# Performance work log

Hardware: AMD Instinct MI355X
Metric: run time of the kernel (lower is better)

## Reference

```python
import jax, jax.numpy as jnp
import numpy as np

B, N, IN, HID, OUT = 64, 256, 7, 64, 32
DEG = 32
NT = B * N          # total nodes per side
E = NT * DEG        # intra-graph edges per side
TAU = 1.0
MAX_ITER = 10
EPS = 1e-5          # InstanceNorm2d eps


def setup_inputs() -> dict:
    key = jax.random.key(0)
    ks = jax.random.split(key, 12)

    def edges(k):
        # random intra-graph edges: local indices in [0, N) plus per-graph offset
        loc = jax.random.randint(k, (2, B, N * DEG), 0, N)
        off = (jnp.arange(B) * N)[None, :, None]
        return (loc + off).reshape(2, -1).astype(jnp.int64)

    def lin(k, fi, fo):
        return jax.random.normal(k, (fi, fo), jnp.float32) / np.float32(np.sqrt(fi))

    return {
        "x1": jax.random.normal(ks[0], (NT, IN), jnp.float32),
        "x2": jax.random.normal(ks[1], (NT, IN), jnp.float32),
        "edge1": edges(ks[2]),
        "edge2": edges(ks[3]),
        "Wl1": lin(ks[4], IN, HID), "Wr1": lin(ks[5], IN, HID),
        "bl1": jnp.zeros((HID,), jnp.float32), "br1": jnp.zeros((HID,), jnp.float32),
        "att1": jax.random.normal(ks[6], (HID,), jnp.float32) * 0.1,
        "bias1": jnp.zeros((HID,), jnp.float32),
        "Wl2": lin(ks[7], HID, OUT), "Wr2": lin(ks[8], HID, OUT),
        "bl2": jnp.zeros((OUT,), jnp.float32), "br2": jnp.zeros((OUT,), jnp.float32),
        "att2": jax.random.normal(ks[9], (OUT,), jnp.float32) * 0.1,
        "bias2": jnp.zeros((OUT,), jnp.float32),
        "gamma": jnp.ones((1,), jnp.float32),
        "beta": jnp.zeros((1,), jnp.float32),
    }


def _gatv2(x, src, dst, Wl, bl, Wr, br, att, bias):
    # PyG GATv2Conv, heads=1: score = att . leaky_relu(lin_l(x_j) + lin_r(x_i))
    xl = x @ Wl + bl  # source transform
    xr = x @ Wr + br  # target transform
    e = jax.nn.leaky_relu(xl[src] + xr[dst], 0.2)     # [E, D]
    score = e @ att                                    # [E]
    smax = jax.ops.segment_max(score, dst, num_segments=NT)
    ex = jnp.exp(score - smax[dst])
    den = jax.ops.segment_sum(ex, dst, num_segments=NT)
    alpha = ex / den[dst]
    out = jax.ops.segment_sum(alpha[:, None] * xl[src], dst, num_segments=NT)
    return out + bias


def _encode(x, edge, params):
    # add self loops (PyG add_self_loops=True default)
    loops = jnp.arange(NT)
    src = jnp.concatenate([edge[0], loops])
    dst = jnp.concatenate([edge[1], loops])
    h = jax.nn.relu(_gatv2(x, src, dst, *params[0]))
    return _gatv2(h, src, dst, *params[1])


def _soft_topk(sim_n):
    # AFAT-style differentiable top-k: OT between flattened scores and
    # {min, max} anchors with marginals [(n-k)/n, k/n], k = N2 per pair.
    n = N * N
    k = N
    flat = sim_n.reshape(B, n)
    mn = flat.min(axis=1, keepdims=True)
    mx = flat.max(axis=1, keepdims=True)
    dist = jnp.stack([flat - mn, mx - flat], axis=-1)  # [B, n, 2] (|s-min|,|s-max|)
    logK = -dist / TAU
    log_row = -jnp.log(jnp.float32(n))
    log_col = jnp.log(jnp.array([(n - k) / n, k / n], jnp.float32))
    for i in range(MAX_ITER):
        if i % 2 == 0:  # row normalization to uniform 1/n
            logK = logK - jax.scipy.special.logsumexp(logK, axis=-1, keepdims=True) + log_row
        else:           # column normalization to [(n-k)/n, k/n]
            logK = logK - jax.scipy.special.logsumexp(logK, axis=1, keepdims=True) + log_col[None, None, :]
    soft = jnp.clip(jnp.exp(logK[:, :, 1]) * n, 0.0, 1.0)  # selection probability per entry
    return soft.reshape(B, N, N)


def reference(x1, x2, edge1, edge2, Wl1, Wr1, bl1, br1, att1, bias1,
              Wl2, Wr2, bl2, br2, att2, bias2, gamma, beta):
    params = ((Wl1, bl1, Wr1, br1, att1, bias1), (Wl2, bl2, Wr2, br2, att2, bias2))
    h1 = _encode(x1, edge1, params).reshape(B, N, OUT)
    h2 = _encode(x2, edge2, params).reshape(B, N, OUT)
    sim = jnp.einsum('bnd,bmd->bnm', h1, h2)
    # InstanceNorm2d(1, affine=True): normalize each pair's sim matrix
    mu = sim.mean(axis=(1, 2), keepdims=True)
    var = sim.var(axis=(1, 2), keepdims=True)
    sim_n = gamma[0] * (sim - mu) * jax.lax.rsqrt(var + EPS) + beta[0]
    return _soft_topk(sim_n)  # soft_S stacked over the batch, [B, N, N]
```

## Files before the change

kernel.cpp:

```cpp
#include <hip/hip_runtime.h>

#define NB 64
#define NN 256
#define IND 7
#define HIDD 64
#define OUTD 32
#define EPG 8192
#define ETOT 524288
#define CAPQ 2600
#define SRCPAD 2624

typedef _Float16 f16;
typedef f16 f16x2 __attribute__((ext_vector_type(2)));
typedef f16 f16x4 __attribute__((ext_vector_type(4)));
typedef f16 f16x8 __attribute__((ext_vector_type(8)));
typedef float f32x4 __attribute__((ext_vector_type(4)));

__device__ __forceinline__ float bsum16(float v, float* rb){
#pragma unroll
  for (int o = 32; o > 0; o >>= 1) v += __shfl_xor(v, o, 64);
  __syncthreads();
  if ((threadIdx.x & 63) == 0) rb[threadIdx.x >> 6] = v;
  __syncthreads();
  float s = 0.f;
#pragma unroll
  for (int i = 0; i < 16; i++) s += rb[i];
  return s;
}
__device__ __forceinline__ float bmin16(float v, float* rb){
#pragma unroll
  for (int o = 32; o > 0; o >>= 1) v = fminf(v, __shfl_xor(v, o, 64));
  __syncthreads();
  if ((threadIdx.x & 63) == 0) rb[threadIdx.x >> 6] = v;
  __syncthreads();
  float s = rb[0];
#pragma unroll
  for (int i = 1; i < 16; i++) s = fminf(s, rb[i]);
  return s;
}
__device__ __forceinline__ float bmax16(float v, float* rb){
#pragma unroll
  for (int o = 32; o > 0; o >>= 1) v = fmaxf(v, __shfl_xor(v, o, 64));
  __syncthreads();
  if ((threadIdx.x & 63) == 0) rb[threadIdx.x >> 6] = v;
  __syncthreads();
  float s = rb[0];
#pragma unroll
  for (int i = 1; i < 16; i++) s = fmaxf(s, rb[i]);
  return s;
}

__device__ __forceinline__ f16x2 lrelu2(f16x2 s){
  const f16x2 k = {(f16)0.2f, (f16)0.2f};
  return __builtin_elementwise_max(s, s * k);
}
__device__ __forceinline__ f16x2 shfl_h2(f16x2 v, int lane){
  int i = __builtin_bit_cast(int, v);
  i = __shfl(i, lane, 64);
  return __builtin_bit_cast(f16x2, i);
}
__device__ __forceinline__ unsigned fkey(float f){
  unsigned b = __float_as_uint(f);
  return (b & 0x80000000u) ? ~b : (b | 0x80000000u);
}
__device__ __forceinline__ float fkinv(unsigned k){
  unsigned b = (k & 0x80000000u) ? (k ^ 0x80000000u) : ~k;
  return __uint_as_float(b);
}

__global__ __launch_bounds__(512, 4) void gat1(
    const float* __restrict__ x1, const float* __restrict__ x2,
    const int* __restrict__ e1, const int* __restrict__ e2,
    const float* __restrict__ Wl, const float* __restrict__ Wr,
    const float* __restrict__ bl, const float* __restrict__ br,
    const float* __restrict__ att, const float* __restrict__ bias,
    f16* __restrict__ hmid,
    int* __restrict__ meta, unsigned char* __restrict__ srcs)
{
  __shared__ __align__(16) f16 xl_s[256 * 72];
  __shared__ float sc_s[CAPQ];
  __shared__ unsigned int src_su[SRCPAD / 4];
  __shared__ int deg_s[64], start_s[64], cnt_s[64];
  __shared__ unsigned char perm[64];
  unsigned char* src_s = (unsigned char*)src_su;

  const int bid = blockIdx.x;
  const int gs = bid >> 2, lo = (bid & 3) * 64;
  const int side = gs >> 6, g = gs & 63;
  const float* x = side ? x2 : x1;
  const int* eb = side ? e2 : e1;
  const int* es = eb + g * EPG;
  const int* ed = eb + ETOT + g * EPG;
  const int t = threadIdx.x;

  if (t < 64) deg_s[t] = 0;

  unsigned short epk[17];
  int nE = 0;
#pragma unroll
  for (int i = 0; i < 17; i++){
    int e = t + i * 512;
    if (e < EPG + 256){
      int sl, dl;
      if (e < EPG){ sl = es[e] & 255; dl = ed[e] & 255; }
      else { sl = dl = e - EPG; }
      epk[i] = (unsigned short)((dl << 8) | sl);
      nE = i + 1;
    }
  }

  {
    const int node = t >> 1, dh = t & 1;
    float xv[IND];
    const float* xr_ = x + (g * 256 + node) * IND;
#pragma unroll
    for (int k = 0; k < IND; k++) xv[k] = xr_[k];
#pragma unroll
    for (int ch = 0; ch < 4; ch++){
      f16x8 o;
#pragma unroll
      for (int j = 0; j < 8; j++){
        int dd = dh * 32 + ch * 8 + j;
        float a = bl[dd];
#pragma unroll
        for (int k = 0; k < IND; k++) a = fmaf(xv[k], Wl[k * HIDD + dd], a);
        o[j] = (f16)a;
      }
      *(f16x8*)&xl_s[node * 72 + dh * 32 + ch * 8] = o;
    }
  }
  __syncthreads();

#pragma unroll
  for (int i = 0; i < 17; i++) if (i < nE){
    int r = (epk[i] >> 8) - lo;
    if ((unsigned)r < 64u) atomicAdd(&deg_s[r], 1);
  }
  __syncthreads();
  if (t < 64){
    int v = deg_s[t], s = v;
#pragma unroll
    for (int off = 1; off < 64; off <<= 1){
      int u = __shfl_up(s, off, 64);
      if (t >= off) s += u;
    }
    start_s[t] = s - v;
    cnt_s[t] = s - v;
    meta[bid * 128 + t] = s - v;
    meta[bid * 128 + 64 + t] = v;
    int r = 0;
#pragma unroll 8
    for (int j = 0; j < 64; j++){
      int dj = deg_s[j];
      r += (dj < v) || (dj == v && j < t);
    }
    perm[r] = (unsigned char)t;
  }
  __syncthreads();
#pragma unroll
  for (int i = 0; i < 17; i++) if (i < nE){
    int dl = epk[i] >> 8, r = dl - lo;
    if ((unsigned)r < 64u){
      int p = atomicAdd(&cnt_s[r], 1);
      if (p < CAPQ) src_s[p] = (unsigned char)(epk[i] & 255);
    }
  }
  __syncthreads();
  {
    int ttl = start_s[63] + deg_s[63];
    if (ttl > CAPQ) ttl = CAPQ;
    unsigned int* gsrc = (unsigned int*)(srcs + (size_t)bid * SRCPAD);
    int nw = (ttl + 3) >> 2;
    for (int i = t; i < nw; i += 512) gsrc[i] = src_su[i];
  }

  const int pairi = perm[t >> 3], sub = t & 7, ln = lo + pairi;
  f16x2 m[4], am[4];
  {
    float xv[IND];
    const float* xq = x + (g * 256 + ln) * IND;
#pragma unroll
    for (int k = 0; k < IND; k++) xv[k] = xq[k];
#pragma unroll
    for (int c = 0; c < 4; c++){
#pragma unroll
      for (int u = 0; u < 2; u++){
        int dd = sub * 8 + 2 * c + u;
        float a = br[dd];
#pragma unroll
        for (int k = 0; k < IND; k++) a = fmaf(xv[k], Wr[k * HIDD + dd], a);
        m[c][u] = (f16)a;
        am[c][u] = (f16)att[dd];
      }
    }
  }
  f16x2 xrh[32], atth[32];
  {
    const int base = (t & 63) & ~7;
#pragma unroll
    for (int ss = 0; ss < 8; ss++){
#pragma unroll
      for (int c = 0; c < 4; c++){
        xrh[ss * 4 + c] = shfl_h2(m[c], base + ss);
        atth[ss * 4 + c] = shfl_h2(am[c], base + ss);
      }
    }
  }

  const int s0 = start_s[pairi];
  int sE = s0 + deg_s[pairi];
  if (sE > CAPQ) sE = CAPQ;
  float lmax = -3.0e38f;
  for (int idx = s0 + sub; idx < sE; idx += 8){
    int sl = src_s[idx];
    const f16x8* rp = (const f16x8*)&xl_s[(unsigned)sl * 72];
    float accs[4] = {0.f, 0.f, 0.f, 0.f};
#pragma unroll
    for (int blk = 0; blk < 8; blk++){
      f16x8 rv = rp[blk];
#pragma unroll
      for (int u = 0; u < 4; u++){
        f16x2 v = {rv[2 * u], rv[2 * u + 1]};
        v = v + xrh[blk * 4 + u];
        accs[u] = __builtin_amdgcn_fdot2(lrelu2(v), atth[blk * 4 + u], accs[u], false);
      }
    }
    float sc = (accs[0] + accs[1]) + (accs[2] + accs[3]);
    sc_s[idx] = sc;
    lmax = fmaxf(lmax, sc);
  }
  lmax = fmaxf(lmax, __shfl_xor(lmax, 1, 64));
  lmax = fmaxf(lmax, __shfl_xor(lmax, 2, 64));
  lmax = fmaxf(lmax, __shfl_xor(lmax, 4, 64));
  const float smax = lmax;
  float ssum = 0.f;
  for (int idx = s0 + sub; idx < sE; idx += 8){
    float w = __expf(sc_s[idx] - smax);
    ssum += w;
    sc_s[idx] = w;
  }
  ssum += __shfl_xor(ssum, 1, 64);
  ssum += __shfl_xor(ssum, 2, 64);
  ssum += __shfl_xor(ssum, 4, 64);
  float inv = 1.f / ssum;
  float acc[8];
#pragma unroll
  for (int c = 0; c < 8; c++) acc[c] = 0.f;
  {
    int sl = (s0 < sE) ? src_s[s0] : 0;
    f16x8 row = *(const f16x8*)&xl_s[(unsigned)sl * 72 + sub * 8];
    for (int idx = s0; idx < sE; idx++){
      int sln = (idx + 1 < sE) ? src_s[idx + 1] : 0;
      f16x8 rown = *(const f16x8*)&xl_s[(unsigned)sln * 72 + sub * 8];
      float w = sc_s[idx];
#pragma unroll
      for (int c = 0; c < 8; c++) acc[c] = fmaf(w, (float)row[c], acc[c]);
      row = rown;
    }
  }
  f16x8 o;
#pragma unroll
  for (int c = 0; c < 8; c++)
    o[c] = (f16)fmaxf(acc[c] * inv + bias[sub * 8 + c], 0.f);
  *(f16x8*)(hmid + (size_t)(gs * 256 + ln) * 64 + sub * 8) = o;
}

__global__ __launch_bounds__(512, 4) void gat2(
    const int* __restrict__ meta, const unsigned char* __restrict__ srcs,
    const f16* __restrict__ hmid,
    const float* __restrict__ Wl, const float* __restrict__ Wr,
    const float* __restrict__ bl, const float* __restrict__ br,
    const float* __restrict__ att, const float* __restrict__ bias,
    f16* __restrict__ hout)
{
  __shared__ __align__(16) f16 xl_s[256 * 40];
  __shared__ __align__(16) f16 xr_s[64 * 40];
  __shared__ float sc_s[CAPQ];
  __shared__ unsigned int src_su[SRCPAD / 4];
  __shared__ int start_s[64], deg_s[64];
  __shared__ unsigned char perm[64];
  unsigned char* src_s = (unsigned char*)src_su;

  const int bid = blockIdx.x;
  const int gs = bid >> 2, lo = (bid & 3) * 64;
  const int t = threadIdx.x;

  if (t < 64){
    start_s[t] = meta[bid * 128 + t];
    deg_s[t] = meta[bid * 128 + 64 + t];
  }
  {
    int ttl = meta[bid * 128 + 63] + meta[bid * 128 + 64 + 63];
    if (ttl > CAPQ) ttl = CAPQ;
    const unsigned int* gsrc = (const unsigned int*)(srcs + (size_t)bid * SRCPAD);
    int nw = (ttl + 3) >> 2;
    for (int i = t; i < nw; i += 512) src_su[i] = gsrc[i];
  }

  {
    const int w = t >> 6, lane = t & 63;
    const int m = lane & 15, quad = lane >> 4;
    f16x8 a[2][2];
#pragma unroll
    for (int ti = 0; ti < 2; ti++){
      const f16* arow = hmid + (size_t)(gs * 256 + (2 * w + ti) * 16 + m) * 64;
      a[ti][0] = *(const f16x8*)(arow + quad * 8);
      a[ti][1] = *(const f16x8*)(arow + 32 + quad * 8);
    }
#pragma unroll
    for (int H = 0; H < 2; H++){
      const int n = H * 16 + m;
      f16x8 b0, b1;
#pragma unroll
      for (int j = 0; j < 8; j++){
        b0[j] = (f16)Wl[(quad * 8 + j) * 32 + n];
        b1[j] = (f16)Wl[(32 + quad * 8 + j) * 32 + n];
      }
      const float bv = bl[n];
#pragma unroll
      for (int ti = 0; ti < 2; ti++){
        f32x4 acc = {0.f, 0.f, 0.f, 0.f};
        acc = __builtin_amdgcn_mfma_f32_16x16x32_f16(a[ti][0], b0, acc, 0, 0, 0);
        acc = __builtin_amdgcn_mfma_f32_16x16x32_f16(a[ti][1], b1, acc, 0, 0, 0);
#pragma unroll
        for (int r = 0; r < 4; r++)
          xl_s[((2 * w + ti) * 16 + quad * 4 + r) * 40 + n] = (f16)(acc[r] + bv);
      }
    }
    if (w < 4){
      const f16* arow = hmid + (size_t)(gs * 256 + lo + w * 16 + m) * 64;
      f16x8 c0 = *(const f16x8*)(arow + quad * 8);
      f16x8 c1 = *(const f16x8*)(arow + 32 + quad * 8);
#pragma unroll
      for (int H = 0; H < 2; H++){
        const int n = H * 16 + m;
        f16x8 b0, b1;
#pragma unroll
        for (int j = 0; j < 8; j++){
          b0[j] = (f16)Wr[(quad * 8 + j) * 32 + n];
          b1[j] = (f16)Wr[(32 + quad * 8 + j) * 32 + n];
        }
        const float bv = br[n];
        f32x4 acc = {0.f, 0.f, 0.f, 0.f};
        acc = __builtin_amdgcn_mfma_f32_16x16x32_f16(c0, b0, acc, 0, 0, 0);
        acc = __builtin_amdgcn_mfma_f32_16x16x32_f16(c1, b1, acc, 0, 0, 0);
#pragma unroll
        for (int r = 0; r < 4; r++)
          xr_s[(w * 16 + quad * 4 + r) * 40 + n] = (f16)(acc[r] + bv);
      }
    }
  }
  __syncthreads();
  if (t < 64){
    int v = deg_s[t], r = 0;
#pragma unroll 8
    for (int j = 0; j < 64; j++){
      int dj = deg_s[j];
      r += (dj < v) || (dj == v && j < t);
    }
    perm[r] = (unsigned char)t;
  }
  __syncthreads();

  const int pairi = perm[t >> 3], sub = t & 7, ln = lo + pairi;
  f16x2 xrh[16], atth[16];
  {
    const f16x8* xrp = (const f16x8*)&xr_s[pairi * 40];
#pragma unroll
    for (int q = 0; q < 4; q++){
      f16x8 v = xrp[q];
#pragma unroll
      for (int u = 0; u < 4; u++){
        xrh[q * 4 + u][0] = v[2 * u];
        xrh[q * 4 + u][1] = v[2 * u + 1];
      }
    }
#pragma unroll
    for (int i = 0; i < 16; i++){
      atth[i][0] = (f16)att[2 * i];
      atth[i][1] = (f16)att[2 * i + 1];
    }
  }

  const int s0 = start_s[pairi];
  int sE = s0 + deg_s[pairi];
  if (sE > CAPQ) sE = CAPQ;
  float lmax = -3.0e38f;
  for (int idx = s0 + sub; idx < sE; idx += 8){
    int sl = src_s[idx];
    const f16x8* rp = (const f16x8*)&xl_s[(unsigned)sl * 40];
    float accs[4] = {0.f, 0.f, 0.f, 0.f};
#pragma unroll
    for (int blk = 0; blk < 4; blk++){
      f16x8 rv = rp[blk];
#pragma unroll
      for (int u = 0; u < 4; u++){
        f16x2 v = {rv[2 * u], rv[2 * u + 1]};
        v = v + xrh[blk * 4 + u];
        accs[u] = __builtin_amdgcn_fdot2(lrelu2(v), atth[blk * 4 + u], accs[u], false);
      }
    }
    float sc = (accs[0] + accs[1]) + (accs[2] + accs[3]);
    sc_s[idx] = sc;
    lmax = fmaxf(lmax, sc);
  }
  lmax = fmaxf(lmax, __shfl_xor(lmax, 1, 64));
  lmax = fmaxf(lmax, __shfl_xor(lmax, 2, 64));
  lmax = fmaxf(lmax, __shfl_xor(lmax, 4, 64));
  const float smax = lmax;
  float ssum = 0.f;
  for (int idx = s0 + sub; idx < sE; idx += 8){
    float w = __expf(sc_s[idx] - smax);
    ssum += w;
    sc_s[idx] = w;
  }
  ssum += __shfl_xor(ssum, 1, 64);
  ssum += __shfl_xor(ssum, 2, 64);
  ssum += __shfl_xor(ssum, 4, 64);
  float inv = 1.f / ssum;

  float acc[4];
#pragma unroll
  for (int c = 0; c < 4; c++) acc[c] = 0.f;
  {
    int sl = (s0 < sE) ? src_s[s0] : 0;
    f16x4 row = *(const f16x4*)&xl_s[(unsigned)sl * 40 + sub * 4];
    for (int idx = s0; idx < sE; idx++){
      int sln = (idx + 1 < sE) ? src_s[idx + 1] : 0;
      f16x4 rown = *(const f16x4*)&xl_s[(unsigned)sln * 40 + sub * 4];
      float w = sc_s[idx];
#pragma unroll
      for (int c = 0; c < 4; c++) acc[c] = fmaf(w, (float)row[c], acc[c]);
      row = rown;
    }
  }
  f16x4 o;
#pragma unroll
  for (int c = 0; c < 4; c++)
    o[c] = (f16)(acc[c] * inv + bias[sub * 4 + c]);
  *(f16x4*)(hout + (size_t)(gs * 256 + ln) * 32 + sub * 4) = o;
}

__global__ __launch_bounds__(256) void zerok(unsigned* __restrict__ stats){
  int i = threadIdx.x;
  if (i < 256) stats[i] = ((i & 3) == 2) ? 0xFFFFFFFFu : 0u;
}

__global__ __launch_bounds__(1024) void simk(
    const f16* __restrict__ H, float* __restrict__ out,
    unsigned* __restrict__ stats)
{
  __shared__ float rb[16];
  const int b = blockIdx.x >> 2, q = blockIdx.x & 3, t = threadIdx.x;
  const int w = t >> 6, lane = t & 63;
  const int m = lane & 15, quad = lane >> 4;
  const int rowT = q * 64 + (w & 3) * 16;
  const int colB = (w >> 2) * 64;

  const f16* h1 = H + (size_t)b * 256 * 32;
  const f16* h2 = H + (size_t)(64 + b) * 256 * 32;

  f16x8 av = *(const f16x8*)(h1 + (size_t)(rowT + m) * 32 + quad * 8);
  f32x4 c[4];
#pragma unroll
  for (int jj = 0; jj < 4; jj++){
    f16x8 bv = *(const f16x8*)(h2 + (size_t)(colB + jj * 16 + m) * 32 + quad * 8);
    f32x4 z = {0.f, 0.f, 0.f, 0.f};
    c[jj] = __builtin_amdgcn_mfma_f32_16x16x32_f16(av, bv, z, 0, 0, 0);
  }

  float sm = 0.f, s2 = 0.f, mn = 3.0e38f, mx = -3.0e38f;
  float* ob = out + (size_t)b * 65536;
#pragma unroll
  for (int jj = 0; jj < 4; jj++)
#pragma unroll
    for (int r = 0; r < 4; r++){
      float s = c[jj][r];
      sm += s; s2 = fmaf(s, s, s2);
      mn = fminf(mn, s); mx = fmaxf(mx, s);
      ob[(rowT + quad * 4 + r) * 256 + colB + jj * 16 + m] = s;
    }
  sm = bsum16(sm, rb);
  s2 = bsum16(s2, rb);
  mn = bmin16(mn, rb);
  mx = bmax16(mx, rb);
  if (t == 0){
    atomicAdd((float*)&stats[b * 4 + 0], sm);
    atomicAdd((float*)&stats[b * 4 + 1], s2);
    atomicMin(&stats[b * 4 + 2], fkey(mn));
    atomicMax(&stats[b * 4 + 3], fkey(mx));
  }
}

__global__ __launch_bounds__(1024) void sinkk(
    const float* __restrict__ sim, const unsigned* __restrict__ stats,
    const float* __restrict__ gamma, const float* __restrict__ beta,
    float* __restrict__ res)
{
  __shared__ float rb[16];
  __shared__ unsigned int hist[8192];
  const int b = blockIdx.x, t = threadIdx.x;

  const float sum = __uint_as_float(stats[b * 4 + 0]);
  const float ssq = __uint_as_float(stats[b * 4 + 1]);
  const float mn = fkinv(stats[b * 4 + 2]);
  const float mx = fkinv(stats[b * 4 + 3]);

  const float mu = sum * (1.f / 65536.f);
  const float var = ssq * (1.f / 65536.f) - mu * mu;
  const float a = gamma[0] * rsqrtf(var + 1e-5f);
  const float cc = beta[0] - a * mu;
  float mnn = a * mn + cc, mxn = a * mx + cc;
  if (a < 0.f){ float tmp = mnn; mnn = mxn; mxn = tmp; }
  const float al = 2.f * a;
  const float be = 2.f * cc - mnn - mxn;
  const float R = fmaxf(mxn - mnn, 1e-12f);
  const float binscale = 4096.f / R;

  for (int i = t; i < 8192; i += 1024) hist[i] = 0u;
  __syncthreads();
  const f32x4* sp = (const f32x4*)(sim + (size_t)b * 65536);
#pragma unroll
  for (int k = 0; k < 16; k++){
    f32x4 v = sp[k * 1024 + t];
#pragma unroll
    for (int u = 0; u < 4; u++){
      float z = fmaf(al, v[u], be);
      int bi = (int)fmaf(z, binscale, 4096.f);
      bi = min(max(bi, 0), 8191);
      atomicAdd(&hist[bi], 1u);
    }
  }
  __syncthreads();

  const float wbin = R * (1.f / 4096.f);
  float ebs[8], cnts[8];
#pragma unroll
  for (int j = 0; j < 8; j++){
    float zc = fmaf((float)(t * 8 + j) + 0.5f, wbin, -R);
    ebs[j] = __expf(-zc);
    cnts[j] = (float)hist[t * 8 + j];
  }

  float D = 0.f, S = 256.f, eD = 1.f;
  for (int p = 0; p < 5; p++){
    float loc = 0.f;
#pragma unroll
    for (int j = 0; j < 8; j++)
      loc += cnts[j] / (1.f + ebs[j] * eD);
    S = bsum16(loc, rb);
    if (p < 4){
      D += -5.5412635f  + __logf(65536.f - S) - __logf(S);
      eD = __expf(-D);
    }
  }
  if (t == 0){
    res[b * 4 + 0] = al;
    res[b * 4 + 1] = be + D;
    res[b * 4 + 2] = 256.f / S;
  }
}

__global__ __launch_bounds__(256) void outk(
    float* __restrict__ out, const float* __restrict__ res)
{
  const int b = blockIdx.x >> 3, seg = blockIdx.x & 7, t = threadIdx.x;
  const float al = res[b * 4 + 0];
  const float beD = res[b * 4 + 1];
  const float scale = res[b * 4 + 2];
  f32x4* p = (f32x4*)(out + (size_t)b * 65536 + seg * 8192);
#pragma unroll
  for (int k = 0; k < 8; k++){
    f32x4 v = p[k * 256 + t];
#pragma unroll
    for (int u = 0; u < 4; u++){
      float z = fmaf(al, v[u], beD);
      v[u] = fminf(scale / (1.f + __expf(-z)), 1.f);
    }
    p[k * 256 + t] = v;
  }
}

extern "C" void kernel_launch(void* const* d_in, const int* in_sizes, int n_in,
                              void* d_out, int out_size, void* d_ws, size_t ws_size,
                              hipStream_t stream)
{
  const float* x1   = (const float*)d_in[0];
  const float* x2   = (const float*)d_in[1];
  const int*   e1   = (const int*)d_in[2];
  const int*   e2   = (const int*)d_in[3];
  const float* Wl1  = (const float*)d_in[4];
  const float* Wr1  = (const float*)d_in[5];
  const float* bl1  = (const float*)d_in[6];
  const float* br1  = (const float*)d_in[7];
  const float* att1 = (const float*)d_in[8];
  const float* bias1= (const float*)d_in[9];
  const float* Wl2  = (const float*)d_in[10];
  const float* Wr2  = (const float*)d_in[11];
  const float* bl2  = (const float*)d_in[12];
  const float* br2  = (const float*)d_in[13];
  const float* att2 = (const float*)d_in[14];
  const float* bias2= (const float*)d_in[15];
  const float* gamma= (const float*)d_in[16];
  const float* beta = (const float*)d_in[17];

  char* ws = (char*)d_ws;
  f16* hmid = (f16*)ws;
  f16* hfin = (f16*)(ws + (size_t)4 * 1024 * 1024);
  int* meta = (int*)(ws + (size_t)6 * 1024 * 1024);
  unsigned char* srcs = (unsigned char*)(ws + (size_t)6 * 1024 * 1024 + 512 * 128 * 4);
  unsigned* stats = (unsigned*)(ws + (size_t)8 * 1024 * 1024);
  float* res = (float*)(ws + (size_t)8 * 1024 * 1024 + 4096);
  float* out = (float*)d_out;

  zerok<<<1, 256, 0, stream>>>(stats);
  gat1<<<512, 512, 0, stream>>>(x1, x2, e1, e2, Wl1, Wr1, bl1, br1, att1, bias1,
                                hmid, meta, srcs);
  gat2<<<512, 512, 0, stream>>>(meta, srcs, hmid, Wl2, Wr2, bl2, br2, att2, bias2, hfin);
  simk<<<256, 1024, 0, stream>>>(hfin, out, stats);
  sinkk<<<64, 1024, 0, stream>>>(out, stats, gamma, beta, res);
  outk<<<512, 256, 0, stream>>>(out, res);
}
```

Baseline: 190.8 us.

## Fuse sinkhorn solve with output pass, store sim in fp16, drop zero kernel

Stats initialisation moves into the first GAT kernel, so the separate zeroing launch goes away. The similarity matrix is written to workspace as fp16 instead of into the fp32 output, which halves that intermediate traffic. The sinkhorn kernel now keeps exp(-z) per element in registers and writes the final clipped sigmoid itself, removing the separate output kernel and its read-modify-write of the full output. In exchange, sim values lose precision in fp16, each thread holds 64 extra registers, and the 16MB output write now comes from only 64 blocks rather than 512.

After: 188.1 us. Within noise of the previous version (-1.4%).

```diff
diff --git a/kernel.cpp b/kernel.cpp
--- a/kernel.cpp
+++ b/kernel.cpp
@@ -75,7 +75,8 @@
     const float* __restrict__ bl, const float* __restrict__ br,
     const float* __restrict__ att, const float* __restrict__ bias,
     f16* __restrict__ hmid,
-    int* __restrict__ meta, unsigned char* __restrict__ srcs)
+    int* __restrict__ meta, unsigned char* __restrict__ srcs,
+    unsigned* __restrict__ stats)
 {
   __shared__ __align__(16) f16 xl_s[256 * 72];
   __shared__ float sc_s[CAPQ];
@@ -92,6 +93,8 @@
   const int* es = eb + g * EPG;
   const int* ed = eb + ETOT + g * EPG;
   const int t = threadIdx.x;
+
+  if (bid == 0 && t < 256) stats[t] = ((t & 3) == 2) ? 0xFFFFFFFFu : 0u;
 
   if (t < 64) deg_s[t] = 0;
 
@@ -441,13 +444,8 @@
   *(f16x4*)(hout + (size_t)(gs * 256 + ln) * 32 + sub * 4) = o;
 }
 
-__global__ __launch_bounds__(256) void zerok(unsigned* __restrict__ stats){
-  int i = threadIdx.x;
-  if (i < 256) stats[i] = ((i & 3) == 2) ? 0xFFFFFFFFu : 0u;
-}
-
 __global__ __launch_bounds__(1024) void simk(
-    const f16* __restrict__ H, float* __restrict__ out,
+    const f16* __restrict__ H, f16* __restrict__ simh,
     unsigned* __restrict__ stats)
 {
   __shared__ float rb[16];
@@ -470,7 +468,7 @@
   }
 
   float sm = 0.f, s2 = 0.f, mn = 3.0e38f, mx = -3.0e38f;
-  float* ob = out + (size_t)b * 65536;
+  f16* ob = simh + (size_t)b * 65536;
 #pragma unroll
   for (int jj = 0; jj < 4; jj++)
 #pragma unroll
@@ -478,7 +476,7 @@
       float s = c[jj][r];
       sm += s; s2 = fmaf(s, s, s2);
       mn = fminf(mn, s); mx = fmaxf(mx, s);
-      ob[(rowT + quad * 4 + r) * 256 + colB + jj * 16 + m] = s;
+      ob[(rowT + quad * 4 + r) * 256 + colB + jj * 16 + m] = (f16)s;
     }
   sm = bsum16(sm, rb);
   s2 = bsum16(s2, rb);
@@ -492,10 +490,10 @@
   }
 }
 
-__global__ __launch_bounds__(1024) void sinkk(
-    const float* __restrict__ sim, const unsigned* __restrict__ stats,
+__global__ __launch_bounds__(1024) void sinkoutk(
+    const f16* __restrict__ simh, const unsigned* __restrict__ stats,
     const float* __restrict__ gamma, const float* __restrict__ beta,
-    float* __restrict__ res)
+    float* __restrict__ out)
 {
   __shared__ float rb[16];
   __shared__ unsigned int hist[8192];
@@ -519,16 +517,18 @@
 
   for (int i = t; i < 8192; i += 1024) hist[i] = 0u;
   __syncthreads();
-  const f32x4* sp = (const f32x4*)(sim + (size_t)b * 65536);
-#pragma unroll
-  for (int k = 0; k < 16; k++){
-    f32x4 v = sp[k * 1024 + t];
-#pragma unroll
-    for (int u = 0; u < 4; u++){
-      float z = fmaf(al, v[u], be);
+  const f16x8* sp = (const f16x8*)(simh + (size_t)b * 65536);
+  float ez[64];
+#pragma unroll
+  for (int ch = 0; ch < 8; ch++){
+    f16x8 v = sp[ch * 1024 + t];
+#pragma unroll
+    for (int u = 0; u < 8; u++){
+      float z = fmaf(al, (float)v[u], be);
       int bi = (int)fmaf(z, binscale, 4096.f);
       bi = min(max(bi, 0), 8191);
       atomicAdd(&hist[bi], 1u);
+      ez[ch * 8 + u] = __expf(-z);
     }
   }
   __syncthreads();
@@ -554,30 +554,19 @@
       eD = __expf(-D);
     }
   }
-  if (t == 0){
-    res[b * 4 + 0] = al;
-    res[b * 4 + 1] = be + D;
-    res[b * 4 + 2] = 256.f / S;
-  }
-}
-
-__global__ __launch_bounds__(256) void outk(
-    float* __restrict__ out, const float* __restrict__ res)
-{
-  const int b = blockIdx.x >> 3, seg = blockIdx.x & 7, t = threadIdx.x;
-  const float al = res[b * 4 + 0];
-  const float beD = res[b * 4 + 1];
-  const float scale = res[b * 4 + 2];
-  f32x4* p = (f32x4*)(out + (size_t)b * 65536 + seg * 8192);
-#pragma unroll
-  for (int k = 0; k < 8; k++){
-    f32x4 v = p[k * 256 + t];
+
+  const float scale = 256.f / S;
+  f32x4* ob = (f32x4*)(out + (size_t)b * 65536);
+#pragma unroll
+  for (int ch = 0; ch < 8; ch++){
+    f32x4 o0, o1;
 #pragma unroll
     for (int u = 0; u < 4; u++){
-      float z = fmaf(al, v[u], beD);
-      v[u] = fminf(scale / (1.f + __expf(-z)), 1.f);
-    }
-    p[k * 256 + t] = v;
+      o0[u] = fminf(scale / (1.f + ez[ch * 8 + u] * eD), 1.f);
+      o1[u] = fminf(scale / (1.f + ez[ch * 8 + 4 + u] * eD), 1.f);
+    }
+    ob[(ch * 1024 + t) * 2] = o0;
+    ob[(ch * 1024 + t) * 2 + 1] = o1;
   }
 }
 
@@ -605,19 +594,17 @@
   const float* beta = (const float*)d_in[17];
 
   char* ws = (char*)d_ws;
-  f16* hmid = (f16*)ws;
-  f16* hfin = (f16*)(ws + (size_t)4 * 1024 * 1024);
+  f16* hfin = (f16*)ws;
+  f16* hmid = (f16*)(ws + (size_t)2 * 1024 * 1024);
   int* meta = (int*)(ws + (size_t)6 * 1024 * 1024);
   unsigned char* srcs = (unsigned char*)(ws + (size_t)6 * 1024 * 1024 + 512 * 128 * 4);
-  unsigned* stats = (unsigned*)(ws + (size_t)8 * 1024 * 1024);
-  float* res = (float*)(ws + (size_t)8 * 1024 * 1024 + 4096);
+  f16* simh = (f16*)(ws + (size_t)2 * 1024 * 1024);
+  unsigned* stats = (unsigned*)(ws + (size_t)10 * 1024 * 1024);
   float* out = (float*)d_out;
 
-  zerok<<<1, 256, 0, stream>>>(stats);
   gat1<<<512, 512, 0, stream>>>(x1, x2, e1, e2, Wl1, Wr1, bl1, br1, att1, bias1,
-                                hmid, meta, srcs);
+                                hmid, meta, srcs, stats);
   gat2<<<512, 512, 0, stream>>>(meta, srcs, hmid, Wl2, Wr2, bl2, br2, att2, bias2, hfin);
-  simk<<<256, 1024, 0, stream>>>(hfin, out, stats);
-  sinkk<<<64, 1024, 0, stream>>>(out, stats, gamma, beta, res);
-  outk<<<512, 256, 0, stream>>>(out, res);
-}
+  simk<<<256, 1024, 0, stream>>>(hfin, simh, stats);
+  sinkoutk<<<64, 1024, 0, stream>>>(simh, stats, gamma, beta, out);
+}
```
